# Performance work log

Hardware: AMD Instinct MI355X
Metric: run time of the kernel (lower is better)

## Reference

```python
import jax, jax.numpy as jnp
import numpy as np

W_BLEND, L1, L2, L3 = 0.5, 0.3, 0.3, 0.4
B, S, F, H, C = 64, 256, 256, 1024, 256


def setup_inputs() -> dict:
    key = jax.random.key(0)
    ks = jax.random.split(key, 11)
    sc = 0.05  # keep recurrence numerically tame
    return {
        "x": jax.random.normal(ks[0], (B, S, F), jnp.float32),
        "W_ih0": jax.random.normal(ks[1], (4 * H, 2 * F), jnp.float32) * sc,
        "W_hh0": jax.random.normal(ks[2], (4 * H, H), jnp.float32) * sc,
        "b_ih0": jax.random.normal(ks[3], (4 * H,), jnp.float32) * sc,
        "b_hh0": jax.random.normal(ks[4], (4 * H,), jnp.float32) * sc,
        "W_ih1": jax.random.normal(ks[5], (4 * H, H), jnp.float32) * sc,
        "W_hh1": jax.random.normal(ks[6], (4 * H, H), jnp.float32) * sc,
        "b_ih1": jax.random.normal(ks[7], (4 * H,), jnp.float32) * sc,
        "b_hh1": jax.random.normal(ks[8], (4 * H,), jnp.float32) * sc,
        "fc_W": jax.random.normal(ks[9], (C, H), jnp.float32) * sc,
        "fc_b": jax.random.normal(ks[10], (C,), jnp.float32) * sc,
    }


def _lstm_cell(inp, h, c, W_ih, W_hh, b_ih, b_hh):
    # PyTorch gate order: i, f, g, o
    gates = inp @ W_ih.T + h @ W_hh.T + b_ih + b_hh  # [B, 4H]
    i, f, g, o = jnp.split(gates, 4, axis=-1)
    i, f, o = jax.nn.sigmoid(i), jax.nn.sigmoid(f), jax.nn.sigmoid(o)
    g = jnp.tanh(g)
    c_new = f * c + i * g
    h_new = o * jnp.tanh(c_new)
    return h_new, c_new


def reference(x, W_ih0, W_hh0, b_ih0, b_hh0, W_ih1, W_hh1, b_ih1, b_hh1, fc_W, fc_b):
    Bx = x.shape[0]
    denom = 1.0 + W_BLEND * (L1 + L2 + L3)
    h0 = jnp.zeros((Bx, H), x.dtype)
    c0 = jnp.zeros((Bx, H), x.dtype)
    action0 = jnp.zeros((Bx, F), x.dtype)

    def step(carry, inputs):
        h0_, c0_, h1_, c1_, action = carry
        x_t, idx = inputs  # x_t: [B, F]
        inp = jnp.concatenate([x_t, action], axis=-1)  # [B, 2F]
        h0n, c0n = _lstm_cell(inp, h0_, c0_, W_ih0, W_hh0, b_ih0, b_hh0)
        h1n, c1n = _lstm_cell(h0n, h1_, c1_, W_ih1, W_hh1, b_ih1, b_hh1)
        out = h1n @ fc_W.T + fc_b  # [B, C] == [B, F]
        blend = ((1.0 + W_BLEND * L2) * x_t + W_BLEND * L1 * action
                 + W_BLEND * L3 * out) / denom
        new_action = jnp.where(idx < 1, x_t, blend)
        return (h0n, c0n, h1n, c1n, new_action), new_action

    xs = (jnp.swapaxes(x, 0, 1), jnp.arange(x.shape[1]))  # ([S,B,F], [S])
    _, actions = jax.lax.scan(step, (h0, c0, h0, c0, action0), xs)
    return jnp.swapaxes(actions, 0, 1)  # [B, S, F]
```

## Files before the change

kernel.cpp:

```cpp
#include <hip/hip_runtime.h>

#define B_ 64
#define S_ 256
#define F_ 256
#define H_ 1024

typedef __attribute__((ext_vector_type(8))) short bf16x8;
typedef __attribute__((ext_vector_type(4))) float f32x4;
typedef unsigned long long u64;

#define MFMA(a, b, c) __builtin_amdgcn_mfma_f32_16x16x32_bf16(a, b, c, 0, 0, 0)
#define CBAR() asm volatile("" ::: "memory")

__device__ __forceinline__ float sig(float v) { return 1.0f / (1.0f + __expf(-v)); }
__device__ __forceinline__ float tanh_(float v) { return 1.0f - 2.0f / (__expf(2.0f * v) + 1.0f); }
__device__ __forceinline__ short bfr(float f) {
    unsigned u = __float_as_uint(f);
    u += 0x7fffu + ((u >> 16) & 1u);
    return (short)(u >> 16);
}

__device__ __forceinline__ void st4(short* base, size_t byteoff, unsigned v) {
    __hip_atomic_store((unsigned*)((char*)base + byteoff), v,
                       __ATOMIC_RELAXED, __HIP_MEMORY_SCOPE_AGENT);
}

__device__ __forceinline__ void flag_add(unsigned* line) {
    asm volatile("s_waitcnt vmcnt(0)" ::: "memory");
    __hip_atomic_fetch_add(line, 1u, __ATOMIC_RELAXED, __HIP_MEMORY_SCOPE_AGENT);
}

__device__ __forceinline__ void flag_wait_g(unsigned* lines, int lane31, unsigned tgt) {
    for (;;) {
        unsigned s = __hip_atomic_load(&lines[lane31 * 16], __ATOMIC_RELAXED,
                                       __HIP_MEMORY_SCOPE_AGENT);
        s += __shfl_xor(s, 1);
        s += __shfl_xor(s, 2);
        s += __shfl_xor(s, 4);
        s += __shfl_xor(s, 8);
        s += __shfl_xor(s, 16);
        if (s >= tgt) break;
        __builtin_amdgcn_s_sleep(1);
    }
    CBAR();
}

__device__ __forceinline__ void rel_wait(unsigned* f, unsigned tgt) {
    while (__hip_atomic_load(f, __ATOMIC_RELAXED, __HIP_MEMORY_SCOPE_AGENT) < tgt)
        __builtin_amdgcn_s_sleep(1);
    CBAR();
}

__device__ __forceinline__ void tok_spin(volatile unsigned* tk, unsigned v) {
    while (*tk < v) __builtin_amdgcn_s_sleep(1);
    CBAR();
}

__global__ __launch_bounds__(256) void conv_x(const float* __restrict__ x,
                                              short* __restrict__ xbf) {
    int tid = blockIdx.x * 256 + threadIdx.x;
    int lane = tid & 63;
    int m = (tid >> 6) & 3;
    int kf = (tid >> 8) & 7;
    int t = tid >> 11;
    int b = m * 16 + (lane & 15);
    int kb = kf * 32 + (lane >> 4) * 8;
    const float* src = x + ((size_t)b * S_ + t) * F_ + kb;
    float4 v0 = *(const float4*)src, v1 = *(const float4*)(src + 4);
    bf16x8 o;
    o[0] = bfr(v0.x); o[1] = bfr(v0.y); o[2] = bfr(v0.z); o[3] = bfr(v0.w);
    o[4] = bfr(v1.x); o[5] = bfr(v1.y); o[6] = bfr(v1.z); o[7] = bfr(v1.w);
    *(bf16x8*)(xbf + (size_t)tid * 8) = o;
}

__global__ void zero_f(float* __restrict__ p, int n) {
    int i = blockIdx.x * blockDim.x + threadIdx.x;
    if (i < n) p[i] = 0.0f;
}

__global__ __launch_bounds__(256) void precomp(const float* __restrict__ Wih0,
                                               const float* __restrict__ fcW,
                                               const float* __restrict__ fcb,
                                               short* __restrict__ Mf,
                                               float* __restrict__ c0ws) {
    __shared__ float WaL[16][256];
    const int nf = blockIdx.x, tid = threadIdx.x;
    #pragma unroll
    for (int r = 0; r < 16; ++r) {
        int rowp = nf * 16 + r;
        int up = rowp >> 2, gat = rowp & 3;
        WaL[r][tid] = Wih0[(size_t)(gat * H_ + up) * 512 + 256 + tid];
    }
    __syncthreads();
    f32x4 acc[16];
    #pragma unroll
    for (int r = 0; r < 16; ++r) acc[r] = (f32x4){0, 0, 0, 0};
    for (int c = 0; c < 256; ++c) {
        f32x4 wv = *(const f32x4*)&fcW[(size_t)c * 1024 + tid * 4];
        #pragma unroll
        for (int r = 0; r < 16; ++r) acc[r] += WaL[r][c] * wv;
    }
    #pragma unroll
    for (int r = 0; r < 16; ++r) {
        #pragma unroll
        for (int jj = 0; jj < 4; ++jj) {
            int h = tid * 4 + jj;
            int kf = h >> 5;
            int lane = r + ((h >> 3) & 3) * 16;
            int j = h & 7;
            Mf[((size_t)nf * 32 + kf) * 512 + lane * 8 + j] = bfr(acc[r][jj]);
        }
    }
    if (tid < 16) {
        float s = 0.0f;
        for (int c = 0; c < 256; ++c) s += WaL[tid][c] * fcb[c];
        c0ws[nf * 16 + tid] = s;
    }
}

#define GATES(v)                                                        \
    float x1 = __shfl_xor((v), 1), x2 = __shfl_xor((v), 2), x3 = __shfl_xor((v), 3); \
    float aL = g1 ? x1 : (v), aH = g1 ? x3 : x2;                        \
    float bL = g1 ? (v) : x1, bH = g1 ? x2 : x3;                        \
    float i_ = g2 ? aH : aL;                                            \
    float f_ = g2 ? bH : bL;                                            \
    float gc = g2 ? aL : aH;                                            \
    float o_ = g2 ? bL : bH;                                            \
    i_ = sig(i_); f_ = sig(f_); o_ = sig(o_); gc = tanh_(gc);

__global__ __launch_bounds__(512, 1) void persist(
    const float* __restrict__ Wih0, const float* __restrict__ Whh0,
    const float* __restrict__ bih0, const float* __restrict__ bhh0,
    const float* __restrict__ Wih1, const float* __restrict__ Whh1,
    const float* __restrict__ bih1, const float* __restrict__ bhh1,
    const float* __restrict__ fcW,  const float* __restrict__ fcb,
    const float* __restrict__ x,    const short* __restrict__ xbf,
    short* __restrict__ h0S, short* __restrict__ h1S,
    const short* __restrict__ Mf, const float* __restrict__ c0ws,
    float* __restrict__ outp,
    unsigned* __restrict__ flagA, unsigned* __restrict__ flagB,
    unsigned* __restrict__ relA,  unsigned* __restrict__ relB)
{
    __shared__ f32x4 red[2048];
    __shared__ f32x4 fcred[256];
    __shared__ short ldsC[16384];
    __shared__ unsigned tokA, tokB;
    const int tid = threadIdx.x, lane = tid & 63, w = tid >> 6;
    const int nf = blockIdx.x;
    const int lane31 = lane & 31;
    unsigned* lineA = &flagA[(nf >> 3) * 16];
    unsigned* lineB = &flagB[(nf >> 3) * 16];
    unsigned* myRelA = &relA[(nf >> 5) * 16];
    unsigned* myRelB = &relB[(nf >> 5) * 16];
    const int rowp = nf * 16 + (lane & 15);
    const int up = rowp >> 2, g = rowp & 3;
    const int g1 = lane & 1, g2 = lane & 2;
    const f32x4 zero4 = {0, 0, 0, 0};
    const int chunkA = (nf >> 3) * 4 + w;
    const int lsBase = ((nf & 7) >> 1) * 16;
    const int pb = (nf & 1) * 4 + ((lane & 15) >> 3) * 2;
    const int mfc = nf >> 4;

    if (tid == 0) { tokA = 0; tokB = 0; }

    bf16x8 wA[5];
    {
        int k = w * 32 + (lane >> 4) * 8;
        const float* src = Wih0 + (size_t)(g * H_ + up) * 512 + k;
        #pragma unroll
        for (int j = 0; j < 8; ++j) wA[0][j] = bfr(src[j]);
    }
    #pragma unroll
    for (int i = 1; i < 5; ++i) {
        int kh = (w * 4 + (i - 1)) * 32 + (lane >> 4) * 8;
        const float* src = Whh0 + (size_t)(g * H_ + up) * 1024 + kh;
        #pragma unroll
        for (int j = 0; j < 8; ++j) wA[i][j] = bfr(src[j]);
    }
    bf16x8 waQ;
    {
        int k = 256 + w * 32 + (lane >> 4) * 8;
        const float* src = Wih0 + (size_t)(g * H_ + up) * 512 + k;
        #pragma unroll
        for (int j = 0; j < 8; ++j) waQ[j] = bfr(src[j]);
    }
    bf16x8 wB[8];
    #pragma unroll
    for (int i = 0; i < 8; ++i) {
        int kf = w * 8 + i;
        int k = kf * 32 + (lane >> 4) * 8;
        const float* src = (k < 1024) ? (Wih1 + (size_t)(g * H_ + up) * 1024 + k)
                                      : (Whh1 + (size_t)(g * H_ + up) * 1024 + (k - 1024));
        #pragma unroll
        for (int j = 0; j < 8; ++j) wB[i][j] = bfr(src[j]);
    }
    bf16x8 wM[4];
    #pragma unroll
    for (int i = 0; i < 4; ++i)
        wM[i] = *(const bf16x8*)(Mf + ((size_t)nf * 32 + (w * 4 + i)) * 512 + lane * 8);
    const float bias0 = bih0[g * H_ + up] + bhh0[g * H_ + up];
    const float bias1 = bih1[g * H_ + up] + bhh1[g * H_ + up];
    const float c0l = c0ws[nf * 16 + (lane & 15)];
    float biasC = 0.0f;
    if (nf < 64) {
        int rowc = (nf & 15) * 16 + (lane & 15);
        biasC = fcb[rowc];
        #pragma unroll
        for (int i = 0; i < 4; ++i) {
            int kf = w * 4 + i;
            int k = kf * 32 + (lane >> 4) * 8;
            const float* src = fcW + (size_t)rowc * 1024 + k;
            short* d = ldsC + ((size_t)kf * 64 + lane) * 8;
            #pragma unroll
            for (int j = 0; j < 8; ++j) d[j] = bfr(src[j]);
        }
    }
    __syncthreads();

    float cs0[4] = {0, 0, 0, 0}, cs1[4] = {0, 0, 0, 0};
    float areg[4] = {0, 0, 0, 0}, P[4] = {0, 0, 0, 0};

    f32x4 ga0, ga1, ga2, ga3, q0, q1, q2, q3;
    f32x4 qp0 = zero4, qp1 = zero4, qp2 = zero4, qp3 = zero4;
    {
        const short* p = xbf + (size_t)w * 2048 + lane * 8;
        bf16x8 a0 = *(const bf16x8*)(p);
        bf16x8 a1 = *(const bf16x8*)(p + 512);
        bf16x8 a2 = *(const bf16x8*)(p + 1024);
        bf16x8 a3 = *(const bf16x8*)(p + 1536);
        ga0 = MFMA(a0, wA[0], zero4);  ga1 = MFMA(a1, wA[0], zero4);
        ga2 = MFMA(a2, wA[0], zero4);  ga3 = MFMA(a3, wA[0], zero4);
        q0 = MFMA(a0, waQ, zero4);  q1 = MFMA(a1, waQ, zero4);
        q2 = MFMA(a2, waQ, zero4);  q3 = MFMA(a3, waQ, zero4);
    }

    for (int t = 0; t < S_; ++t) {
        const unsigned ut = (unsigned)t;
        short* h0w = h0S + (size_t)t * 65536;
        const short* h1r = h1S + (size_t)t * 65536;
        short* h1w = h1S + (size_t)(t + 1) * 65536;

        if (t > 0) {
            if (w == 0) {
                if (nf == 0) {
                    flag_wait_g(flagB, lane31, 256u * ut);
                    if (lane < 8)
                        __hip_atomic_store(&relB[lane * 16], ut,
                                           __ATOMIC_RELAXED, __HIP_MEMORY_SCOPE_AGENT);
                } else {
                    rel_wait(myRelB, ut);
                }
                if (lane == 0) *(volatile unsigned*)&tokB = ut;
                CBAR();
            } else {
                tok_spin(&tokB, ut);
            }
            f32x4 m0 = zero4, m1 = zero4, m2 = zero4, m3 = zero4;
            #pragma unroll
            for (int i = 0; i < 4; ++i) {
                const short* p = h1r + (size_t)(w * 4 + i) * 2048 + lane * 8;
                bf16x8 a0 = *(const bf16x8*)(p);
                bf16x8 a1 = *(const bf16x8*)(p + 512);
                bf16x8 a2 = *(const bf16x8*)(p + 1024);
                bf16x8 a3 = *(const bf16x8*)(p + 1536);
                m0 = MFMA(a0, wM[i], m0);
                m1 = MFMA(a1, wM[i], m1);
                m2 = MFMA(a2, wM[i], m2);
                m3 = MFMA(a3, wM[i], m3);
            }
            f32x4 R0 = (t == 1) ? qp0 : (1.15f * qp0 + 0.2f * m0);
            f32x4 R1 = (t == 1) ? qp1 : (1.15f * qp1 + 0.2f * m1);
            f32x4 R2 = (t == 1) ? qp2 : (1.15f * qp2 + 0.2f * m2);
            f32x4 R3 = (t == 1) ? qp3 : (1.15f * qp3 + 0.2f * m3);
            red[(w * 4 + 0) * 64 + lane] = R0;
            red[(w * 4 + 1) * 64 + lane] = R1;
            red[(w * 4 + 2) * 64 + lane] = R2;
            red[(w * 4 + 3) * 64 + lane] = R3;
            __syncthreads();
            if (w < 4) {
                f32x4 s = red[(0 * 4 + w) * 64 + lane];
                #pragma unroll
                for (int k = 1; k < 8; ++k) s += red[(k * 4 + w) * 64 + lane];
                #pragma unroll
                for (int r = 0; r < 4; ++r)
                    P[r] = (t == 1) ? s[r]
                         : (s[r] + 0.15f * P[r] + 0.2f * c0l) * (1.0f / 1.5f);
            }
            __syncthreads();
        }

        red[(w * 4 + 0) * 64 + lane] = ga0;
        red[(w * 4 + 1) * 64 + lane] = ga1;
        red[(w * 4 + 2) * 64 + lane] = ga2;
        red[(w * 4 + 3) * 64 + lane] = ga3;
        __syncthreads();
        if (w < 4) {
            f32x4 s = red[(0 * 4 + w) * 64 + lane];
            #pragma unroll
            for (int k = 1; k < 8; ++k) s += red[(k * 4 + w) * 64 + lane];
            #pragma unroll
            for (int r = 0; r < 4; ++r) {
                float v = s[r] + bias0 + P[r];
                GATES(v)
                float cn = f_ * cs0[r] + i_ * gc;
                cs0[r] = cn;
                float hn = o_ * tanh_(cn);
                int hv = (int)(unsigned short)bfr(hn);
                int ot = __shfl_xor(hv, 4);
                unsigned p32 = (lane & 4) ? (unsigned)((ot & 0xffff) | (hv << 16))
                                          : (unsigned)((hv & 0xffff) | (ot << 16));
                if ((lane & 7) == 0) {
                    int b = w * 16 + (lane >> 4) * 4 + r;
                    int ls = lsBase + (b & 15);
                    st4(h0w, (size_t)chunkA * 1024 + (size_t)ls * 16 + pb * 2, p32);
                }
            }
        } else if (nf < 64 && t > 0) {
            const int j = w - 4;
            f32x4 f0 = zero4;
            #pragma unroll
            for (int i = 0; i < 8; ++i) {
                const int kf = j * 8 + i;
                const bf16x8 bw = *(const bf16x8*)(ldsC + ((size_t)kf * 64 + lane) * 8);
                bf16x8 a = *(const bf16x8*)(h1r + (size_t)kf * 2048 + (size_t)mfc * 512 + lane * 8);
                f0 = MFMA(a, bw, f0);
            }
            fcred[j * 64 + lane] = f0;
        }
        __syncthreads();
        if (tid == 0) flag_add(lineA);

        f32x4 b0 = zero4, b1 = zero4, b2 = zero4, b3 = zero4;
        if (w == 0) {
            if (nf == 0) {
                flag_wait_g(flagA, lane31, 256u * (ut + 1u));
                if (lane < 8)
                    __hip_atomic_store(&relA[lane * 16], ut + 1u,
                                       __ATOMIC_RELAXED, __HIP_MEMORY_SCOPE_AGENT);
            } else {
                rel_wait(myRelA, ut + 1u);
            }
            if (lane == 0) *(volatile unsigned*)&tokA = ut + 1u;
            CBAR();
        } else if (w < 4) {
            tok_spin(&tokA, ut + 1u);
        } else if (w == 4 && nf < 64 && t > 0) {
            f32x4 s = fcred[lane];
            s += fcred[64 + lane];
            s += fcred[128 + lane];
            s += fcred[192 + lane];
            const int c = (nf & 15) * 16 + (lane & 15);
            #pragma unroll
            for (int r = 0; r < 4; ++r) {
                float ov = s[r] + biasC;
                int b = mfc * 16 + (lane >> 4) * 4 + r;
                size_t xi = ((size_t)b * S_ + (t - 1)) * F_ + c;
                float xv = x[xi];
                float na = (t == 1) ? xv
                         : (1.15f * xv + 0.15f * areg[r] + 0.2f * ov) * (1.0f / 1.5f);
                areg[r] = na;
                outp[xi] = na;
            }
        }
        #pragma unroll
        for (int i = 0; i < 8; ++i) {
            const int kf = w * 8 + i;
            const short* p = (kf < 32) ? (h0w + (size_t)kf * 2048 + lane * 8)
                                       : (h1r + (size_t)(kf - 32) * 2048 + lane * 8);
            bf16x8 a0 = *(const bf16x8*)(p);
            bf16x8 a1 = *(const bf16x8*)(p + 512);
            bf16x8 a2 = *(const bf16x8*)(p + 1024);
            bf16x8 a3 = *(const bf16x8*)(p + 1536);
            b0 = MFMA(a0, wB[i], b0);
            b1 = MFMA(a1, wB[i], b1);
            b2 = MFMA(a2, wB[i], b2);
            b3 = MFMA(a3, wB[i], b3);
        }
        red[(w * 4 + 0) * 64 + lane] = b0;
        red[(w * 4 + 1) * 64 + lane] = b1;
        red[(w * 4 + 2) * 64 + lane] = b2;
        red[(w * 4 + 3) * 64 + lane] = b3;
        __syncthreads();
        if (w < 4) {
            f32x4 s = red[(0 * 4 + w) * 64 + lane];
            #pragma unroll
            for (int k = 1; k < 8; ++k) s += red[(k * 4 + w) * 64 + lane];
            #pragma unroll
            for (int r = 0; r < 4; ++r) {
                float v = s[r] + bias1;
                GATES(v)
                float cn = f_ * cs1[r] + i_ * gc;
                cs1[r] = cn;
                float hn = o_ * tanh_(cn);
                int hv = (int)(unsigned short)bfr(hn);
                int ot = __shfl_xor(hv, 4);
                unsigned p32 = (lane & 4) ? (unsigned)((ot & 0xffff) | (hv << 16))
                                          : (unsigned)((hv & 0xffff) | (ot << 16));
                if ((lane & 7) == 0) {
                    int b = w * 16 + (lane >> 4) * 4 + r;
                    int ls = lsBase + (b & 15);
                    st4(h1w, (size_t)chunkA * 1024 + (size_t)ls * 16 + pb * 2, p32);
                }
            }
        }
        __syncthreads();
        if (tid == 0) flag_add(lineB);

        if (t < S_ - 1) {
            qp0 = q0; qp1 = q1; qp2 = q2; qp3 = q3;
            const short* p = xbf + (size_t)(t + 1) * 16384 + (size_t)w * 2048 + lane * 8;
            bf16x8 a0 = *(const bf16x8*)(p);
            bf16x8 a1 = *(const bf16x8*)(p + 512);
            bf16x8 a2 = *(const bf16x8*)(p + 1024);
            bf16x8 a3 = *(const bf16x8*)(p + 1536);
            ga0 = MFMA(a0, wA[0], zero4);  ga1 = MFMA(a1, wA[0], zero4);
            ga2 = MFMA(a2, wA[0], zero4);  ga3 = MFMA(a3, wA[0], zero4);
            q0 = MFMA(a0, waQ, zero4);  q1 = MFMA(a1, waQ, zero4);
            q2 = MFMA(a2, waQ, zero4);  q3 = MFMA(a3, waQ, zero4);
            #pragma unroll
            for (int i = 1; i < 5; ++i) {
                const short* ph = h0w + (size_t)(w * 4 + (i - 1)) * 2048 + lane * 8;
                bf16x8 h0f = *(const bf16x8*)(ph);
                bf16x8 h1f = *(const bf16x8*)(ph + 512);
                bf16x8 h2f = *(const bf16x8*)(ph + 1024);
                bf16x8 h3f = *(const bf16x8*)(ph + 1536);
                ga0 = MFMA(h0f, wA[i], ga0);
                ga1 = MFMA(h1f, wA[i], ga1);
                ga2 = MFMA(h2f, wA[i], ga2);
                ga3 = MFMA(h3f, wA[i], ga3);
            }
        }
    }

    if (nf < 64) {
        if (w == 0) {
            if (nf == 0) {
                flag_wait_g(flagB, lane31, 256u * 256u);
                if (lane < 8)
                    __hip_atomic_store(&relB[lane * 16], 256u,
                                       __ATOMIC_RELAXED, __HIP_MEMORY_SCOPE_AGENT);
            } else {
                rel_wait(myRelB, 256u);
            }
            if (lane == 0) *(volatile unsigned*)&tokB = 256u;
            CBAR();
        } else {
            tok_spin(&tokB, 256u);
        }
        const short* h1f = h1S + (size_t)256 * 65536;
        if (w >= 4) {
            const int j = w - 4;
            f32x4 f0 = zero4;
            #pragma unroll
            for (int i = 0; i < 8; ++i) {
                const int kf = j * 8 + i;
                const bf16x8 bw = *(const bf16x8*)(ldsC + ((size_t)kf * 64 + lane) * 8);
                bf16x8 a = *(const bf16x8*)(h1f + (size_t)kf * 2048 + (size_t)mfc * 512 + lane * 8);
                f0 = MFMA(a, bw, f0);
            }
            fcred[j * 64 + lane] = f0;
        }
        __syncthreads();
        if (w == 4) {
            f32x4 s = fcred[lane];
            s += fcred[64 + lane];
            s += fcred[128 + lane];
            s += fcred[192 + lane];
            const int c = (nf & 15) * 16 + (lane & 15);
            #pragma unroll
            for (int r = 0; r < 4; ++r) {
                float ov = s[r] + biasC;
                int b = mfc * 16 + (lane >> 4) * 4 + r;
                size_t xi = ((size_t)b * S_ + (S_ - 1)) * F_ + c;
                float xv = x[xi];
                float na = (1.15f * xv + 0.15f * areg[r] + 0.2f * ov) * (1.0f / 1.5f);
                outp[xi] = na;
            }
        }
    }
}

extern "C" void kernel_launch(void* const* d_in, const int* in_sizes, int n_in,
                              void* d_out, int out_size, void* d_ws, size_t ws_size,
                              hipStream_t stream) {
    const float* x    = (const float*)d_in[0];
    const float* Wih0 = (const float*)d_in[1];
    const float* Whh0 = (const float*)d_in[2];
    const float* bih0 = (const float*)d_in[3];
    const float* bhh0 = (const float*)d_in[4];
    const float* Wih1 = (const float*)d_in[5];
    const float* Whh1 = (const float*)d_in[6];
    const float* bih1 = (const float*)d_in[7];
    const float* bhh1 = (const float*)d_in[8];
    const float* fcW  = (const float*)d_in[9];
    const float* fcb  = (const float*)d_in[10];
    float* outp = (float*)d_out;

    char* ws = (char*)d_ws;
    short* xbf   = (short*)(ws + 0);
    short* Mf    = (short*)(ws + 8388608);
    float* c0ws  = (float*)(ws + 16777216);
    unsigned* flagA = (unsigned*)(ws + 16793600);
    unsigned* flagB = (unsigned*)(ws + 16795648);
    unsigned* relA  = (unsigned*)(ws + 16797696);
    unsigned* relB  = (unsigned*)(ws + 16798208);
    short* h0S   = (short*)(ws + 16798720);
    short* h1S   = (short*)(ws + 50353152);

    conv_x<<<2048, 256, 0, stream>>>(x, xbf);
    precomp<<<256, 256, 0, stream>>>(Wih0, fcW, fcb, Mf, c0ws);
    zero_f<<<5, 256, 0, stream>>>((float*)(ws + 16793600), 1280);
    zero_f<<<128, 256, 0, stream>>>((float*)(ws + 50353152), 32768);

    persist<<<256, 512, 0, stream>>>(Wih0, Whh0, bih0, bhh0,
                                     Wih1, Whh1, bih1, bhh1,
                                     fcW, fcb, x, xbf,
                                     h0S, h1S, Mf, c0ws, outp,
                                     flagA, flagB, relA, relB);
}
```

Before: 3.365 ms.

## Repartition waves so layer-0 and layer-1 recurrent GEMMs run in separate phases

```diff
diff --git a/kernel.cpp b/kernel.cpp
--- a/kernel.cpp
+++ b/kernel.cpp
@@ -141,8 +141,10 @@
     unsigned* __restrict__ flagA, unsigned* __restrict__ flagB,
     unsigned* __restrict__ relA,  unsigned* __restrict__ relB)
 {
-    __shared__ f32x4 red[2048];
-    __shared__ f32x4 fcred[256];
+    __shared__ f32x4 redGA[2048];
+    __shared__ f32x4 redBv[2048];
+    __shared__ f32x4 redDv[2048];
+    __shared__ f32x4 fcF[256];
     __shared__ short ldsC[16384];
     __shared__ unsigned tokA, tokB;
     const int tid = threadIdx.x, lane = tid & 63, w = tid >> 6;
@@ -163,41 +165,38 @@
 
     if (tid == 0) { tokA = 0; tokB = 0; }
 
-    bf16x8 wA[5];
+    bf16x8 wA0, waQ, wH[8], wX[8];
     {
         int k = w * 32 + (lane >> 4) * 8;
         const float* src = Wih0 + (size_t)(g * H_ + up) * 512 + k;
         #pragma unroll
-        for (int j = 0; j < 8; ++j) wA[0][j] = bfr(src[j]);
-    }
-    #pragma unroll
-    for (int i = 1; i < 5; ++i) {
-        int kh = (w * 4 + (i - 1)) * 32 + (lane >> 4) * 8;
-        const float* src = Whh0 + (size_t)(g * H_ + up) * 1024 + kh;
-        #pragma unroll
-        for (int j = 0; j < 8; ++j) wA[i][j] = bfr(src[j]);
-    }
-    bf16x8 waQ;
+        for (int j = 0; j < 8; ++j) wA0[j] = bfr(src[j]);
+    }
     {
         int k = 256 + w * 32 + (lane >> 4) * 8;
         const float* src = Wih0 + (size_t)(g * H_ + up) * 512 + k;
         #pragma unroll
         for (int j = 0; j < 8; ++j) waQ[j] = bfr(src[j]);
     }
-    bf16x8 wB[8];
-    #pragma unroll
-    for (int i = 0; i < 8; ++i) {
-        int kf = w * 8 + i;
-        int k = kf * 32 + (lane >> 4) * 8;
-        const float* src = (k < 1024) ? (Wih1 + (size_t)(g * H_ + up) * 1024 + k)
-                                      : (Whh1 + (size_t)(g * H_ + up) * 1024 + (k - 1024));
-        #pragma unroll
-        for (int j = 0; j < 8; ++j) wB[i][j] = bfr(src[j]);
-    }
-    bf16x8 wM[4];
-    #pragma unroll
-    for (int i = 0; i < 4; ++i)
-        wM[i] = *(const bf16x8*)(Mf + ((size_t)nf * 32 + (w * 4 + i)) * 512 + lane * 8);
+    if (w < 4) {
+        #pragma unroll
+        for (int i = 0; i < 8; ++i) {
+            int k = (w * 8 + i) * 32 + (lane >> 4) * 8;
+            const float* sh = Whh0 + (size_t)(g * H_ + up) * 1024 + k;
+            const float* sx = Wih1 + (size_t)(g * H_ + up) * 1024 + k;
+            #pragma unroll
+            for (int j = 0; j < 8; ++j) { wH[i][j] = bfr(sh[j]); wX[i][j] = bfr(sx[j]); }
+        }
+    } else {
+        #pragma unroll
+        for (int i = 0; i < 8; ++i) {
+            int k = ((w - 4) * 8 + i) * 32 + (lane >> 4) * 8;
+            const float* sh = Whh1 + (size_t)(g * H_ + up) * 1024 + k;
+            #pragma unroll
+            for (int j = 0; j < 8; ++j) wH[i][j] = bfr(sh[j]);
+            wX[i] = *(const bf16x8*)(Mf + ((size_t)nf * 32 + (w - 4) * 8 + i) * 512 + lane * 8);
+        }
+    }
     const float bias0 = bih0[g * H_ + up] + bhh0[g * H_ + up];
     const float bias1 = bih1[g * H_ + up] + bhh1[g * H_ + up];
     const float c0l = c0ws[nf * 16 + (lane & 15)];
@@ -228,8 +227,8 @@
         bf16x8 a1 = *(const bf16x8*)(p + 512);
         bf16x8 a2 = *(const bf16x8*)(p + 1024);
         bf16x8 a3 = *(const bf16x8*)(p + 1536);
-        ga0 = MFMA(a0, wA[0], zero4);  ga1 = MFMA(a1, wA[0], zero4);
-        ga2 = MFMA(a2, wA[0], zero4);  ga3 = MFMA(a3, wA[0], zero4);
+        ga0 = MFMA(a0, wA0, zero4);  ga1 = MFMA(a1, wA0, zero4);
+        ga2 = MFMA(a2, wA0, zero4);  ga3 = MFMA(a3, wA0, zero4);
         q0 = MFMA(a0, waQ, zero4);  q1 = MFMA(a1, waQ, zero4);
         q2 = MFMA(a2, waQ, zero4);  q3 = MFMA(a3, waQ, zero4);
     }
@@ -240,8 +239,8 @@
         const short* h1r = h1S + (size_t)t * 65536;
         short* h1w = h1S + (size_t)(t + 1) * 65536;
 
-        if (t > 0) {
-            if (w == 0) {
+        if (w == 0) {
+            if (t > 0) {
                 if (nf == 0) {
                     flag_wait_g(flagB, lane31, 256u * ut);
                     if (lane < 8)
@@ -252,52 +251,71 @@
                 }
                 if (lane == 0) *(volatile unsigned*)&tokB = ut;
                 CBAR();
-            } else {
-                tok_spin(&tokB, ut);
-            }
-            f32x4 m0 = zero4, m1 = zero4, m2 = zero4, m3 = zero4;
-            #pragma unroll
-            for (int i = 0; i < 4; ++i) {
-                const short* p = h1r + (size_t)(w * 4 + i) * 2048 + lane * 8;
+            }
+        } else if (w >= 4 && t > 0) {
+            tok_spin(&tokB, ut);
+        }
+        redGA[(w * 4 + 0) * 64 + lane] = ga0;
+        redGA[(w * 4 + 1) * 64 + lane] = ga1;
+        redGA[(w * 4 + 2) * 64 + lane] = ga2;
+        redGA[(w * 4 + 3) * 64 + lane] = ga3;
+        f32x4 m0 = zero4, m1 = zero4, m2 = zero4, m3 = zero4;
+        if (w >= 4) {
+            f32x4 b0 = zero4, b1 = zero4, b2 = zero4, b3 = zero4;
+            #pragma unroll
+            for (int i = 0; i < 8; ++i) {
+                const short* p = h1r + (size_t)((w - 4) * 8 + i) * 2048 + lane * 8;
                 bf16x8 a0 = *(const bf16x8*)(p);
                 bf16x8 a1 = *(const bf16x8*)(p + 512);
                 bf16x8 a2 = *(const bf16x8*)(p + 1024);
                 bf16x8 a3 = *(const bf16x8*)(p + 1536);
-                m0 = MFMA(a0, wM[i], m0);
-                m1 = MFMA(a1, wM[i], m1);
-                m2 = MFMA(a2, wM[i], m2);
-                m3 = MFMA(a3, wM[i], m3);
-            }
-            f32x4 R0 = (t == 1) ? qp0 : (1.15f * qp0 + 0.2f * m0);
-            f32x4 R1 = (t == 1) ? qp1 : (1.15f * qp1 + 0.2f * m1);
-            f32x4 R2 = (t == 1) ? qp2 : (1.15f * qp2 + 0.2f * m2);
-            f32x4 R3 = (t == 1) ? qp3 : (1.15f * qp3 + 0.2f * m3);
-            red[(w * 4 + 0) * 64 + lane] = R0;
-            red[(w * 4 + 1) * 64 + lane] = R1;
-            red[(w * 4 + 2) * 64 + lane] = R2;
-            red[(w * 4 + 3) * 64 + lane] = R3;
-            __syncthreads();
-            if (w < 4) {
-                f32x4 s = red[(0 * 4 + w) * 64 + lane];
+                if (t > 1) {
+                    m0 = MFMA(a0, wX[i], m0);
+                    m1 = MFMA(a1, wX[i], m1);
+                    m2 = MFMA(a2, wX[i], m2);
+                    m3 = MFMA(a3, wX[i], m3);
+                }
+                b0 = MFMA(a0, wH[i], b0);
+                b1 = MFMA(a1, wH[i], b1);
+                b2 = MFMA(a2, wH[i], b2);
+                b3 = MFMA(a3, wH[i], b3);
+            }
+            redBv[(w * 4 + 0) * 64 + lane] = b0;
+            redBv[(w * 4 + 1) * 64 + lane] = b1;
+            redBv[(w * 4 + 2) * 64 + lane] = b2;
+            redBv[(w * 4 + 3) * 64 + lane] = b3;
+        }
+        if (t > 0) {
+            f32x4 R0, R1, R2, R3;
+            if (t == 1) { R0 = qp0; R1 = qp1; R2 = qp2; R3 = qp3; }
+            else if (w >= 4) {
+                R0 = 1.15f * qp0 + 0.2f * m0;
+                R1 = 1.15f * qp1 + 0.2f * m1;
+                R2 = 1.15f * qp2 + 0.2f * m2;
+                R3 = 1.15f * qp3 + 0.2f * m3;
+            } else {
+                R0 = 1.15f * qp0; R1 = 1.15f * qp1; R2 = 1.15f * qp2; R3 = 1.15f * qp3;
+            }
+            redDv[(w * 4 + 0) * 64 + lane] = R0;
+            redDv[(w * 4 + 1) * 64 + lane] = R1;
+            redDv[(w * 4 + 2) * 64 + lane] = R2;
+            redDv[(w * 4 + 3) * 64 + lane] = R3;
+        }
+        __syncthreads();
+
+        if (w < 4) {
+            if (t > 0) {
+                f32x4 sD = redDv[(0 * 4 + w) * 64 + lane];
                 #pragma unroll
-                for (int k = 1; k < 8; ++k) s += red[(k * 4 + w) * 64 + lane];
+                for (int k = 1; k < 8; ++k) sD += redDv[(k * 4 + w) * 64 + lane];
                 #pragma unroll
                 for (int r = 0; r < 4; ++r)
-                    P[r] = (t == 1) ? s[r]
-                         : (s[r] + 0.15f * P[r] + 0.2f * c0l) * (1.0f / 1.5f);
-            }
-            __syncthreads();
-        }
-
-        red[(w * 4 + 0) * 64 + lane] = ga0;
-        red[(w * 4 + 1) * 64 + lane] = ga1;
-        red[(w * 4 + 2) * 64 + lane] = ga2;
-        red[(w * 4 + 3) * 64 + lane] = ga3;
-        __syncthreads();
-        if (w < 4) {
-            f32x4 s = red[(0 * 4 + w) * 64 + lane];
-            #pragma unroll
-            for (int k = 1; k < 8; ++k) s += red[(k * 4 + w) * 64 + lane];
+                    P[r] = (t == 1) ? sD[r]
+                         : (sD[r] + 0.15f * P[r] + 0.2f * c0l) * (1.0f / 1.5f);
+            }
+            f32x4 s = redGA[(0 * 4 + w) * 64 + lane];
+            #pragma unroll
+            for (int k = 1; k < 8; ++k) s += redGA[(k * 4 + w) * 64 + lane];
             #pragma unroll
             for (int r = 0; r < 4; ++r) {
                 float v = s[r] + bias0 + P[r];
@@ -325,12 +343,11 @@
                 bf16x8 a = *(const bf16x8*)(h1r + (size_t)kf * 2048 + (size_t)mfc * 512 + lane * 8);
                 f0 = MFMA(a, bw, f0);
             }
-            fcred[j * 64 + lane] = f0;
+            fcF[j * 64 + lane] = f0;
         }
         __syncthreads();
         if (tid == 0) flag_add(lineA);
 
-        f32x4 b0 = zero4, b1 = zero4, b2 = zero4, b3 = zero4;
         if (w == 0) {
             if (nf == 0) {
                 flag_wait_g(flagA, lane31, 256u * (ut + 1u));
@@ -345,10 +362,10 @@
         } else if (w < 4) {
             tok_spin(&tokA, ut + 1u);
         } else if (w == 4 && nf < 64 && t > 0) {
-            f32x4 s = fcred[lane];
-            s += fcred[64 + lane];
-            s += fcred[128 + lane];
-            s += fcred[192 + lane];
+            f32x4 s = fcF[lane];
+            s += fcF[64 + lane];
+            s += fcF[128 + lane];
+            s += fcF[192 + lane];
             const int c = (nf & 15) * 16 + (lane & 15);
             #pragma unroll
             for (int r = 0; r < 4; ++r) {
@@ -362,29 +379,37 @@
                 outp[xi] = na;
             }
         }
-        #pragma unroll
-        for (int i = 0; i < 8; ++i) {
-            const int kf = w * 8 + i;
-            const short* p = (kf < 32) ? (h0w + (size_t)kf * 2048 + lane * 8)
-                                       : (h1r + (size_t)(kf - 32) * 2048 + lane * 8);
-            bf16x8 a0 = *(const bf16x8*)(p);
-            bf16x8 a1 = *(const bf16x8*)(p + 512);
-            bf16x8 a2 = *(const bf16x8*)(p + 1024);
-            bf16x8 a3 = *(const bf16x8*)(p + 1536);
-            b0 = MFMA(a0, wB[i], b0);
-            b1 = MFMA(a1, wB[i], b1);
-            b2 = MFMA(a2, wB[i], b2);
-            b3 = MFMA(a3, wB[i], b3);
-        }
-        red[(w * 4 + 0) * 64 + lane] = b0;
-        red[(w * 4 + 1) * 64 + lane] = b1;
-        red[(w * 4 + 2) * 64 + lane] = b2;
-        red[(w * 4 + 3) * 64 + lane] = b3;
+
+        if (w < 4) {
+            f32x4 b0 = zero4, b1 = zero4, b2 = zero4, b3 = zero4;
+            ga0 = zero4; ga1 = zero4; ga2 = zero4; ga3 = zero4;
+            #pragma unroll
+            for (int i = 0; i < 8; ++i) {
+                const short* p = h0w + (size_t)(w * 8 + i) * 2048 + lane * 8;
+                bf16x8 a0 = *(const bf16x8*)(p);
+                bf16x8 a1 = *(const bf16x8*)(p + 512);
+                bf16x8 a2 = *(const bf16x8*)(p + 1024);
+                bf16x8 a3 = *(const bf16x8*)(p + 1536);
+                b0 = MFMA(a0, wX[i], b0);
+                b1 = MFMA(a1, wX[i], b1);
+                b2 = MFMA(a2, wX[i], b2);
+                b3 = MFMA(a3, wX[i], b3);
+                ga0 = MFMA(a0, wH[i], ga0);
+                ga1 = MFMA(a1, wH[i], ga1);
+                ga2 = MFMA(a2, wH[i], ga2);
+                ga3 = MFMA(a3, wH[i], ga3);
+            }
+            redBv[(w * 4 + 0) * 64 + lane] = b0;
+            redBv[(w * 4 + 1) * 64 + lane] = b1;
+            redBv[(w * 4 + 2) * 64 + lane] = b2;
+            redBv[(w * 4 + 3) * 64 + lane] = b3;
+        }
         __syncthreads();
+
         if (w < 4) {
-            f32x4 s = red[(0 * 4 + w) * 64 + lane];
-            #pragma unroll
-            for (int k = 1; k < 8; ++k) s += red[(k * 4 + w) * 64 + lane];
+            f32x4 s = redBv[(0 * 4 + w) * 64 + lane];
+            #pragma unroll
+            for (int k = 1; k < 8; ++k) s += redBv[(k * 4 + w) * 64 + lane];
             #pragma unroll
             for (int r = 0; r < 4; ++r) {
                 float v = s[r] + bias1;
@@ -413,40 +438,30 @@
             bf16x8 a1 = *(const bf16x8*)(p + 512);
             bf16x8 a2 = *(const bf16x8*)(p + 1024);
             bf16x8 a3 = *(const bf16x8*)(p + 1536);
-            ga0 = MFMA(a0, wA[0], zero4);  ga1 = MFMA(a1, wA[0], zero4);
-            ga2 = MFMA(a2, wA[0], zero4);  ga3 = MFMA(a3, wA[0], zero4);
+            ga0 = MFMA(a0, wA0, (w < 4) ? ga0 : zero4);
+            ga1 = MFMA(a1, wA0, (w < 4) ? ga1 : zero4);
+            ga2 = MFMA(a2, wA0, (w < 4) ? ga2 : zero4);
+            ga3 = MFMA(a3, wA0, (w < 4) ? ga3 : zero4);
             q0 = MFMA(a0, waQ, zero4);  q1 = MFMA(a1, waQ, zero4);
             q2 = MFMA(a2, waQ, zero4);  q3 = MFMA(a3, waQ, zero4);
-            #pragma unroll
-            for (int i = 1; i < 5; ++i) {
-                const short* ph = h0w + (size_t)(w * 4 + (i - 1)) * 2048 + lane * 8;
-                bf16x8 h0f = *(const bf16x8*)(ph);
-                bf16x8 h1f = *(const bf16x8*)(ph + 512);
-                bf16x8 h2f = *(const bf16x8*)(ph + 1024);
-                bf16x8 h3f = *(const bf16x8*)(ph + 1536);
-                ga0 = MFMA(h0f, wA[i], ga0);
-                ga1 = MFMA(h1f, wA[i], ga1);
-                ga2 = MFMA(h2f, wA[i], ga2);
-                ga3 = MFMA(h3f, wA[i], ga3);
-            }
-        }
-    }
-
+        }
+    }
+
+    if (w == 0) {
+        if (nf == 0) {
+            flag_wait_g(flagB, lane31, 256u * 256u);
+            if (lane < 8)
+                __hip_atomic_store(&relB[lane * 16], 256u,
+                                   __ATOMIC_RELAXED, __HIP_MEMORY_SCOPE_AGENT);
+        } else {
+            rel_wait(myRelB, 256u);
+        }
+        if (lane == 0) *(volatile unsigned*)&tokB = 256u;
+        CBAR();
+    } else if (w >= 4) {
+        tok_spin(&tokB, 256u);
+    }
     if (nf < 64) {
-        if (w == 0) {
-            if (nf == 0) {
-                flag_wait_g(flagB, lane31, 256u * 256u);
-                if (lane < 8)
-                    __hip_atomic_store(&relB[lane * 16], 256u,
-                                       __ATOMIC_RELAXED, __HIP_MEMORY_SCOPE_AGENT);
-            } else {
-                rel_wait(myRelB, 256u);
-            }
-            if (lane == 0) *(volatile unsigned*)&tokB = 256u;
-            CBAR();
-        } else {
-            tok_spin(&tokB, 256u);
-        }
         const short* h1f = h1S + (size_t)256 * 65536;
         if (w >= 4) {
             const int j = w - 4;
@@ -458,14 +473,14 @@
                 bf16x8 a = *(const bf16x8*)(h1f + (size_t)kf * 2048 + (size_t)mfc * 512 + lane * 8);
                 f0 = MFMA(a, bw, f0);
             }
-            fcred[j * 64 + lane] = f0;
+            fcF[j * 64 + lane] = f0;
         }
         __syncthreads();
         if (w == 4) {
-            f32x4 s = fcred[lane];
-            s += fcred[64 + lane];
-            s += fcred[128 + lane];
-            s += fcred[192 + lane];
+            f32x4 s = fcF[lane];
+            s += fcF[64 + lane];
+            s += fcF[128 + lane];
+            s += fcF[192 + lane];
             const int c = (nf & 15) * 16 + (lane & 15);
             #pragma unroll
             for (int r = 0; r < 4; ++r) {
```

Result: no change. 3.317 ms (-1.4%).
